# Optimization experiments

Measured on AMD Instinct MI355X. Metric: run time of the kernel, lower is better.

Reference implementation:

```python
import jax, jax.numpy as jnp
import numpy as np


def setup_inputs() -> dict:
    key = jax.random.key(0)
    k1, k2, k3 = jax.random.split(key, 3)
    N, D, E = 16384, 4096, 64
    x = jax.random.normal(k1, (N, D), dtype=jnp.float32)
    W = jax.random.normal(k2, (E, D), dtype=jnp.float32) * (1.0 / np.sqrt(D))
    b = jax.random.normal(k3, (E,), dtype=jnp.float32) * 0.01
    return {"x": x, "W": W, "b": b, "top_k": 2}


def reference(x, W, b, top_k):
    # logits: [N, E]
    logits = jnp.einsum('nd,ed->ne', x, W) + b
    top_vals, top_idx = jax.lax.top_k(logits, top_k)          # [N, k]
    top_probs = jax.nn.softmax(top_vals, axis=-1)             # softmax over the k selected logits
    N = logits.shape[0]
    rows = jnp.arange(N)[:, None]                             # [N, 1]
    gates = jnp.zeros_like(logits).at[rows, top_idx].set(top_probs)  # sparse gate tensor [N, E]
    return gates, top_idx
```

## Files before the change

kernel.cpp:

```cpp
#include <hip/hip_runtime.h>
#include <math.h>

typedef _Float16 f16;
typedef _Float16 f16x8 __attribute__((ext_vector_type(8)));
typedef _Float16 f16x4 __attribute__((ext_vector_type(4)));
typedef float    f32x4 __attribute__((ext_vector_type(4)));

constexpr int D_DIM = 4096;
constexpr int E_DIM = 64;
constexpr int BM    = 64;
constexpr int BK    = 64;
constexpr int NT    = 256;
constexpr int LDT   = BK + 8;
constexpr int LDL   = E_DIM + 1;

constexpr float XSCALE  = 8.0f;
constexpr float WSCALE  = 256.0f;
constexpr float UNSCALE = 1.0f / 2048.0f;

__global__ __launch_bounds__(NT) void pack_w(const float* __restrict__ W,
                                             f16* __restrict__ whi,
                                             f16* __restrict__ wlo) {
    const int i = (blockIdx.x * NT + threadIdx.x) * 4;
    const float4 w = *(const float4*)(W + i);
    const float v[4] = {w.x * WSCALE, w.y * WSCALE, w.z * WSCALE, w.w * WSCALE};
    f16x4 hv, lv;
#pragma unroll
    for (int j = 0; j < 4; ++j) {
        const f16 h = (f16)v[j];
        hv[j] = h;
        lv[j] = (f16)(v[j] - (float)h);
    }
    *(f16x4*)(whi + i) = hv;
    *(f16x4*)(wlo + i) = lv;
}

__global__ __launch_bounds__(NT) void gate_kernel(
    const float* __restrict__ x, const f16* __restrict__ whi,
    const f16* __restrict__ wlo, const float* __restrict__ b,
    float* __restrict__ out, int N)
{
    __shared__ alignas(16) f16 sm[4 * BM * LDT];
    f16* Xh = sm;
    f16* Xl = sm + BM * LDT;
    f16* Wh = sm + 2 * BM * LDT;
    f16* Wl = sm + 3 * BM * LDT;

    const int tid  = threadIdx.x;
    const int row0 = blockIdx.x * BM;

    const int ks = tid & 7;
    const int r8 = tid >> 3;

    const int lane = tid & 63;
    const int wv   = tid >> 6;
    const int r0   = wv * 16;
    const int m    = lane & 15;
    const int quad = lane >> 4;

    f32x4 acc[4] = {{0,0,0,0},{0,0,0,0},{0,0,0,0},{0,0,0,0}};

    float4 xr[2][2];
    f16x8 whr[2], wlr[2];

    const float* xblk = x + (size_t)row0 * D_DIM;

    auto load_tile = [&](int t) {
        const int k0 = t * BK;
#pragma unroll
        for (int p = 0; p < 2; ++p) {
            const int r = p * 32 + r8;
            const float* xp = xblk + (size_t)r * D_DIM + k0 + ks * 8;
            xr[p][0] = ((const float4*)xp)[0];
            xr[p][1] = ((const float4*)xp)[1];
            const size_t wo = (size_t)r * D_DIM + k0 + ks * 8;
            whr[p] = *(const f16x8*)(whi + wo);
            wlr[p] = *(const f16x8*)(wlo + wo);
        }
    };
    auto store_tile = [&]() {
#pragma unroll
        for (int p = 0; p < 2; ++p) {
            const int r = p * 32 + r8;
            const float v[8] = {xr[p][0].x * XSCALE, xr[p][0].y * XSCALE,
                                xr[p][0].z * XSCALE, xr[p][0].w * XSCALE,
                                xr[p][1].x * XSCALE, xr[p][1].y * XSCALE,
                                xr[p][1].z * XSCALE, xr[p][1].w * XSCALE};
            f16x8 hv, lv;
#pragma unroll
            for (int j = 0; j < 8; ++j) {
                const f16 h = (f16)v[j];
                hv[j] = h;
                lv[j] = (f16)(v[j] - (float)h);
            }
            *(f16x8*)&Xh[r * LDT + ks * 8] = hv;
            *(f16x8*)&Xl[r * LDT + ks * 8] = lv;
            *(f16x8*)&Wh[r * LDT + ks * 8] = whr[p];
            *(f16x8*)&Wl[r * LDT + ks * 8] = wlr[p];
        }
    };

    load_tile(0);
    store_tile();
    __syncthreads();

    constexpr int KT = D_DIM / BK;
    for (int t = 0; t < KT; ++t) {
        if (t + 1 < KT) load_tile(t + 1);

#pragma unroll
        for (int kk = 0; kk < 2; ++kk) {
            const int ko = kk * 32 + quad * 8;
            const f16x8 ah = *(const f16x8*)&Xh[(r0 + m) * LDT + ko];
            const f16x8 al = *(const f16x8*)&Xl[(r0 + m) * LDT + ko];
#pragma unroll
            for (int ct = 0; ct < 4; ++ct) {
                const f16x8 bh = *(const f16x8*)&Wh[(ct * 16 + m) * LDT + ko];
                const f16x8 bl = *(const f16x8*)&Wl[(ct * 16 + m) * LDT + ko];
                acc[ct] = __builtin_amdgcn_mfma_f32_16x16x32_f16(ah, bh, acc[ct], 0, 0, 0);
                acc[ct] = __builtin_amdgcn_mfma_f32_16x16x32_f16(ah, bl, acc[ct], 0, 0, 0);
                acc[ct] = __builtin_amdgcn_mfma_f32_16x16x32_f16(al, bh, acc[ct], 0, 0, 0);
            }
        }
        __syncthreads();
        if (t + 1 < KT) store_tile();
        __syncthreads();
    }

    float* Ls  = (float*)sm;
    float* aux = Ls + BM * LDL;

#pragma unroll
    for (int ct = 0; ct < 4; ++ct) {
        const int col = ct * 16 + m;
        const float bb = b[col];
#pragma unroll
        for (int reg = 0; reg < 4; ++reg) {
            const int row = r0 + quad * 4 + reg;
            Ls[row * LDL + col] = acc[ct][reg] * UNSCALE + bb;
        }
    }
    __syncthreads();

    if (tid < BM) {
        const float* lr = &Ls[tid * LDL];
        float v1 = -INFINITY, v2 = -INFINITY;
        int i1 = 0, i2 = 0;
        for (int e = 0; e < E_DIM; ++e) {
            const float v = lr[e];
            if (v > v1)      { v2 = v1; i2 = i1; v1 = v; i1 = e; }
            else if (v > v2) { v2 = v;  i2 = e; }
        }
        const float ex = expf(v2 - v1);
        const float dn = 1.0f + ex;
        aux[tid]       = (float)i1;
        aux[64 + tid]  = (float)i2;
        aux[128 + tid] = 1.0f / dn;
        aux[192 + tid] = ex / dn;
        const size_t basei = (size_t)N * E_DIM + (size_t)(row0 + tid) * 2;
        out[basei]     = (float)i1;
        out[basei + 1] = (float)i2;
    }
    __syncthreads();

#pragma unroll
    for (int p = 0; p < 4; ++p) {
        const int f4 = p * 256 + tid;
        const int r  = f4 >> 4;
        const int c4 = f4 & 15;
        const int i1 = (int)aux[r];
        const int i2 = (int)aux[64 + r];
        const float p1 = aux[128 + r];
        const float p2 = aux[192 + r];
        const int e = c4 * 4;
        float4 g;
        g.x = (e + 0 == i1) ? p1 : (e + 0 == i2) ? p2 : 0.0f;
        g.y = (e + 1 == i1) ? p1 : (e + 1 == i2) ? p2 : 0.0f;
        g.z = (e + 2 == i1) ? p1 : (e + 2 == i2) ? p2 : 0.0f;
        g.w = (e + 3 == i1) ? p1 : (e + 3 == i2) ? p2 : 0.0f;
        *(float4*)(out + (size_t)(row0 + r) * E_DIM + e) = g;
    }
}

extern "C" void kernel_launch(void* const* d_in, const int* in_sizes, int n_in,
                              void* d_out, int out_size, void* d_ws, size_t ws_size,
                              hipStream_t stream) {
    const float* x = (const float*)d_in[0];
    const float* W = (const float*)d_in[1];
    const float* b = (const float*)d_in[2];
    float* out = (float*)d_out;
    const int N = in_sizes[0] / D_DIM;

    f16* whi = (f16*)d_ws;
    f16* wlo = whi + (size_t)E_DIM * D_DIM;

    hipLaunchKernelGGL(pack_w, dim3((E_DIM * D_DIM) / (NT * 4)), dim3(NT),
                       0, stream, W, whi, wlo);
    hipLaunchKernelGGL(gate_kernel, dim3(N / BM), dim3(NT),
                       0, stream, x, whi, wlo, b, out, N);
}
```

Before: 405.1 us.

## Split-K the gating GEMM with a separate top-k reduction kernel

Splits the K dimension across up to 4 blocks per row tile, writing fp32 partial logits to workspace, and adds a finishing kernel that sums the partials, adds the bias and does the top-2 softmax scatter. X is now loaded directly into registers in MFMA fragment layout and split into hi/lo halves there, so shared memory holds only the W tiles. This raises the block count from 256 to up to 1024 so the device is better filled, and adds a launch_bounds occupancy hint. The cost is an extra kernel launch and a round trip of the partials through global memory.

```diff
diff --git a/kernel.cpp b/kernel.cpp
--- a/kernel.cpp
+++ b/kernel.cpp
@@ -35,22 +35,24 @@
     *(f16x4*)(wlo + i) = lv;
 }
 
-__global__ __launch_bounds__(NT) void gate_kernel(
+__global__ __launch_bounds__(NT, 4) void gemm_partial(
     const float* __restrict__ x, const f16* __restrict__ whi,
-    const f16* __restrict__ wlo, const float* __restrict__ b,
-    float* __restrict__ out, int N)
+    const f16* __restrict__ wlo, float* __restrict__ partials, int ksplit)
 {
-    __shared__ alignas(16) f16 sm[4 * BM * LDT];
-    f16* Xh = sm;
-    f16* Xl = sm + BM * LDT;
-    f16* Wh = sm + 2 * BM * LDT;
-    f16* Wl = sm + 3 * BM * LDT;
-
-    const int tid  = threadIdx.x;
-    const int row0 = blockIdx.x * BM;
-
-    const int ks = tid & 7;
-    const int r8 = tid >> 3;
+    __shared__ alignas(16) f16 Wh[E_DIM * LDT];
+    __shared__ alignas(16) f16 Wl[E_DIM * LDT];
+
+    const int tid   = threadIdx.x;
+    const int bx    = blockIdx.x;
+    const int tile  = bx / ksplit;
+    const int split = bx % ksplit;
+    const int row0  = tile * BM;
+    const int dk    = D_DIM / ksplit;
+    const int koff  = split * dk;
+    const int KT    = dk / BK;
+
+    const int ks2 = tid & 3;
+    const int we  = tid >> 2;
 
     const int lane = tid & 63;
     const int wv   = tid >> 6;
@@ -60,85 +62,109 @@
 
     f32x4 acc[4] = {{0,0,0,0},{0,0,0,0},{0,0,0,0},{0,0,0,0}};
 
-    float4 xr[2][2];
     f16x8 whr[2], wlr[2];
-
-    const float* xblk = x + (size_t)row0 * D_DIM;
-
-    auto load_tile = [&](int t) {
-        const int k0 = t * BK;
-#pragma unroll
-        for (int p = 0; p < 2; ++p) {
-            const int r = p * 32 + r8;
-            const float* xp = xblk + (size_t)r * D_DIM + k0 + ks * 8;
-            xr[p][0] = ((const float4*)xp)[0];
-            xr[p][1] = ((const float4*)xp)[1];
-            const size_t wo = (size_t)r * D_DIM + k0 + ks * 8;
-            whr[p] = *(const f16x8*)(whi + wo);
-            wlr[p] = *(const f16x8*)(wlo + wo);
-        }
+    auto loadW = [&](int t) {
+        const size_t o = (size_t)we * D_DIM + koff + t * BK + ks2 * 16;
+        whr[0] = *(const f16x8*)(whi + o);
+        whr[1] = *(const f16x8*)(whi + o + 8);
+        wlr[0] = *(const f16x8*)(wlo + o);
+        wlr[1] = *(const f16x8*)(wlo + o + 8);
     };
-    auto store_tile = [&]() {
-#pragma unroll
-        for (int p = 0; p < 2; ++p) {
-            const int r = p * 32 + r8;
-            const float v[8] = {xr[p][0].x * XSCALE, xr[p][0].y * XSCALE,
-                                xr[p][0].z * XSCALE, xr[p][0].w * XSCALE,
-                                xr[p][1].x * XSCALE, xr[p][1].y * XSCALE,
-                                xr[p][1].z * XSCALE, xr[p][1].w * XSCALE};
-            f16x8 hv, lv;
+    auto storeW = [&]() {
+        *(f16x8*)&Wh[we * LDT + ks2 * 16]     = whr[0];
+        *(f16x8*)&Wh[we * LDT + ks2 * 16 + 8] = whr[1];
+        *(f16x8*)&Wl[we * LDT + ks2 * 16]     = wlr[0];
+        *(f16x8*)&Wl[we * LDT + ks2 * 16 + 8] = wlr[1];
+    };
+
+    const float* xrow = x + (size_t)(row0 + r0 + m) * D_DIM + koff + quad * 8;
+
+    float4 xc[2][2], xn[2][2];
+    auto loadX = [&](float4 d[2][2], int t) {
+#pragma unroll
+        for (int kk = 0; kk < 2; ++kk) {
+            const float* p = xrow + t * BK + kk * 32;
+            d[kk][0] = ((const float4*)p)[0];
+            d[kk][1] = ((const float4*)p)[1];
+        }
+    };
+
+    loadW(0);
+    loadX(xc, 0);
+    storeW();
+    __syncthreads();
+
+    for (int t = 0; t < KT; ++t) {
+        if (t + 1 < KT) { loadW(t + 1); loadX(xn, t + 1); }
+
+#pragma unroll
+        for (int kk = 0; kk < 2; ++kk) {
+            const float v[8] = {xc[kk][0].x * XSCALE, xc[kk][0].y * XSCALE,
+                                xc[kk][0].z * XSCALE, xc[kk][0].w * XSCALE,
+                                xc[kk][1].x * XSCALE, xc[kk][1].y * XSCALE,
+                                xc[kk][1].z * XSCALE, xc[kk][1].w * XSCALE};
+            f16x8 ah, al;
 #pragma unroll
             for (int j = 0; j < 8; ++j) {
                 const f16 h = (f16)v[j];
-                hv[j] = h;
-                lv[j] = (f16)(v[j] - (float)h);
+                ah[j] = h;
+                al[j] = (f16)(v[j] - (float)h);
             }
-            *(f16x8*)&Xh[r * LDT + ks * 8] = hv;
-            *(f16x8*)&Xl[r * LDT + ks * 8] = lv;
-            *(f16x8*)&Wh[r * LDT + ks * 8] = whr[p];
-            *(f16x8*)&Wl[r * LDT + ks * 8] = wlr[p];
-        }
-    };
-
-    load_tile(0);
-    store_tile();
-    __syncthreads();
-
-    constexpr int KT = D_DIM / BK;
-    for (int t = 0; t < KT; ++t) {
-        if (t + 1 < KT) load_tile(t + 1);
-
-#pragma unroll
-        for (int kk = 0; kk < 2; ++kk) {
             const int ko = kk * 32 + quad * 8;
-            const f16x8 ah = *(const f16x8*)&Xh[(r0 + m) * LDT + ko];
-            const f16x8 al = *(const f16x8*)&Xl[(r0 + m) * LDT + ko];
 #pragma unroll
             for (int ct = 0; ct < 4; ++ct) {
                 const f16x8 bh = *(const f16x8*)&Wh[(ct * 16 + m) * LDT + ko];
                 const f16x8 bl = *(const f16x8*)&Wl[(ct * 16 + m) * LDT + ko];
                 acc[ct] = __builtin_amdgcn_mfma_f32_16x16x32_f16(ah, bh, acc[ct], 0, 0, 0);
+                acc[ct] = __builtin_amdgcn_mfma_f32_16x16x32_f16(al, bh, acc[ct], 0, 0, 0);
                 acc[ct] = __builtin_amdgcn_mfma_f32_16x16x32_f16(ah, bl, acc[ct], 0, 0, 0);
-                acc[ct] = __builtin_amdgcn_mfma_f32_16x16x32_f16(al, bh, acc[ct], 0, 0, 0);
             }
         }
         __syncthreads();
-        if (t + 1 < KT) store_tile();
+        if (t + 1 < KT) {
+            storeW();
+#pragma unroll
+            for (int kk = 0; kk < 2; ++kk) { xc[kk][0] = xn[kk][0]; xc[kk][1] = xn[kk][1]; }
+        }
         __syncthreads();
     }
 
-    float* Ls  = (float*)sm;
-    float* aux = Ls + BM * LDL;
-
-#pragma unroll
-    for (int ct = 0; ct < 4; ++ct) {
-        const int col = ct * 16 + m;
-        const float bb = b[col];
-#pragma unroll
-        for (int reg = 0; reg < 4; ++reg) {
-            const int row = r0 + quad * 4 + reg;
-            Ls[row * LDL + col] = acc[ct][reg] * UNSCALE + bb;
-        }
+    float* my = partials + (size_t)bx * (BM * E_DIM);
+#pragma unroll
+    for (int ct = 0; ct < 4; ++ct)
+#pragma unroll
+        for (int reg = 0; reg < 4; ++reg)
+            my[(r0 + quad * 4 + reg) * E_DIM + ct * 16 + m] = acc[ct][reg] * UNSCALE;
+}
+
+__global__ __launch_bounds__(NT) void topk_finish_kernel(
+    const float* __restrict__ partials, const float* __restrict__ b,
+    float* __restrict__ out, int ksplit, int N)
+{
+    __shared__ float smem[BM * LDL + 256];
+    float* Ls  = smem;
+    float* aux = smem + BM * LDL;
+
+    const int tid  = threadIdx.x;
+    const int tile = blockIdx.x;
+    const int row0 = tile * BM;
+    const float* base = partials + (size_t)tile * ksplit * (BM * E_DIM);
+
+#pragma unroll
+    for (int p = 0; p < 4; ++p) {
+        const int f4 = p * 256 + tid;
+        const int r  = f4 >> 4;
+        const int c4 = f4 & 15;
+        float4 s = *(const float4*)(base + (size_t)f4 * 4);
+        for (int sp = 1; sp < ksplit; ++sp) {
+            const float4 t4 = *(const float4*)(base + (size_t)sp * (BM * E_DIM) + (size_t)f4 * 4);
+            s.x += t4.x; s.y += t4.y; s.z += t4.z; s.w += t4.w;
+        }
+        const float4 bb = ((const float4*)b)[c4];
+        Ls[r * LDL + c4 * 4 + 0] = s.x + bb.x;
+        Ls[r * LDL + c4 * 4 + 1] = s.y + bb.y;
+        Ls[r * LDL + c4 * 4 + 2] = s.z + bb.z;
+        Ls[r * LDL + c4 * 4 + 3] = s.w + bb.w;
     }
     __syncthreads();
 
@@ -190,12 +216,22 @@
     const float* b = (const float*)d_in[2];
     float* out = (float*)d_out;
     const int N = in_sizes[0] / D_DIM;
+    const int ntiles = N / BM;
 
     f16* whi = (f16*)d_ws;
     f16* wlo = whi + (size_t)E_DIM * D_DIM;
+    float* partials = (float*)(wlo + (size_t)E_DIM * D_DIM);
+
+    const size_t wplanes = 2 * (size_t)E_DIM * D_DIM * sizeof(f16);
+    const size_t pbytes  = (size_t)BM * E_DIM * sizeof(float);
+    int ksplit = 1;
+    if      (ws_size >= wplanes + (size_t)ntiles * 4 * pbytes) ksplit = 4;
+    else if (ws_size >= wplanes + (size_t)ntiles * 2 * pbytes) ksplit = 2;
 
     hipLaunchKernelGGL(pack_w, dim3((E_DIM * D_DIM) / (NT * 4)), dim3(NT),
                        0, stream, W, whi, wlo);
-    hipLaunchKernelGGL(gate_kernel, dim3(N / BM), dim3(NT),
-                       0, stream, x, whi, wlo, b, out, N);
-}
+    hipLaunchKernelGGL(gemm_partial, dim3(ntiles * ksplit), dim3(NT),
+                       0, stream, x, whi, wlo, partials, ksplit);
+    hipLaunchKernelGGL(topk_finish_kernel, dim3(ntiles), dim3(NT),
+                       0, stream, partials, b, out, ksplit, N);
+}
```

After: 390.5 us. -3.6%, faster.
